# Optimization experiments

Hardware: AMD Instinct MI355X
Metric: run time of the kernel (lower is better)

The kernel has to match this reference:

```python
import math
import jax, jax.numpy as jnp
import numpy as np

B, S, D, H = 2, 2048, 1024, 16
DH = D // H
EPS = 1e-5


def setup_inputs() -> dict:
    key = jax.random.key(0)
    ks = jax.random.split(key, 8)
    def lin(k, din, dout):
        return jax.random.normal(k, (din, dout), dtype=jnp.float32) / math.sqrt(din)
    return {
        "x": jax.random.normal(ks[0], (B, S, D), dtype=jnp.float32),
        "attention_mask": jnp.ones((B, S), dtype=jnp.int32),
        "Wq": lin(ks[1], D, D),
        "Wk": lin(ks[2], D, D),
        "Wv": lin(ks[3], D, D),
        "Wo": lin(ks[4], D, D),
        "W1": lin(ks[5], D, 4 * D),
        "W2": lin(ks[6], 2 * D, D),
        "gamma1": jnp.ones((D,), jnp.float32),
        "beta1": jnp.zeros((D,), jnp.float32),
        "gamma2": jnp.ones((D,), jnp.float32),
        "beta2": jnp.zeros((D,), jnp.float32),
    }


def layernorm(x, gamma, beta):
    mu = jnp.mean(x, axis=-1, keepdims=True)
    xc = x - mu
    var = jnp.mean(xc * xc, axis=-1, keepdims=True)
    return gamma * (xc / jnp.sqrt(var + EPS)) + beta


def softmax_last(x):
    x = x - jnp.max(x, axis=-1, keepdims=True)
    e = jnp.exp(x)
    return e / jnp.sum(e, axis=-1, keepdims=True)


def mhsa(x, attention_mask, Wq, Wk, Wv, Wo, causal=True):
    b, s, d = x.shape
    q = (x @ Wq).reshape(b, s, H, DH).transpose(0, 2, 1, 3)  # [b,h,s,dh]
    k = (x @ Wk).reshape(b, s, H, DH).transpose(0, 2, 1, 3)
    v = (x @ Wv).reshape(b, s, H, DH).transpose(0, 2, 1, 3)
    score = jnp.einsum("bhqd,bhkd->bhqk", q, k) / math.sqrt(DH)
    if causal:
        cmask = jnp.tril(jnp.ones((s, s), dtype=bool))
        score = jnp.where(cmask[None, None], score, -jnp.inf)
    key_mask = attention_mask.astype(bool)[:, None, None, :]  # [b,1,1,s]
    score = jnp.where(key_mask, score, -jnp.inf)
    attn = softmax_last(score)
    out = jnp.einsum("bhqk,bhkd->bhqd", attn, v)
    out = out.transpose(0, 2, 1, 3).reshape(b, s, d)
    return out @ Wo


def reference(x, attention_mask, Wq, Wk, Wv, Wo, W1, W2, gamma1, beta1, gamma2, beta2):
    x1 = x + mhsa(layernorm(x, gamma1, beta1), attention_mask, Wq, Wk, Wv, Wo, causal=True)
    h = layernorm(x1, gamma2, beta2) @ W1          # [b,s,4d]
    left, right = h[:, :, : 2 * D], h[:, :, 2 * D :]
    glu = left * jax.nn.sigmoid(right)             # [b,s,2d]
    return x1 + glu @ W2
```

## Files before the change

### kernel.cpp

```cpp
#include <hip/hip_runtime.h>
#include <hip/hip_bf16.h>
#include <math.h>

#define BB 2
#define SS 2048
#define DD 1024
#define HH 16
#define DH 64
#define NTOK (BB * SS)
#define LN_EPS 1e-5f
#define BIGNEG -1e30f

typedef __attribute__((ext_vector_type(8))) short bf16x8;
typedef __attribute__((ext_vector_type(4))) float f32x4;

static __device__ __forceinline__ unsigned short f2bu(float f) {
    __hip_bfloat16 h = __float2bfloat16(f);
    return *(unsigned short*)&h;
}

static __device__ __forceinline__ float fast_exp2(float x) {
    return __builtin_amdgcn_exp2f(x);
}

static __device__ __forceinline__ void async16(const void* g, void* l) {
    __builtin_amdgcn_global_load_lds((const __attribute__((address_space(1))) void*)g,
                                     (__attribute__((address_space(3))) void*)l, 16, 0, 0);
}


__global__ __launch_bounds__(256) void prep_kernel(const float* __restrict__ Wq,
                                                   const float* __restrict__ Wk,
                                                   const float* __restrict__ Wv,
                                                   const float* __restrict__ Wo,
                                                   const float* __restrict__ W1,
                                                   const float* __restrict__ W2,
                                                   __hip_bfloat16* __restrict__ wqkvt,
                                                   __hip_bfloat16* __restrict__ wot,
                                                   __hip_bfloat16* __restrict__ w1t,
                                                   __hip_bfloat16* __restrict__ w2t,
                                                   const float* __restrict__ x,
                                                   const float* __restrict__ gamma,
                                                   const float* __restrict__ beta,
                                                   __hip_bfloat16* __restrict__ lnb) {
    __shared__ float t[32][33];
    __shared__ float red[256];
    const int bid = blockIdx.x;
    const int tid = threadIdx.x;

    if (bid >= 10240) {
        const int row = bid - 10240;
        const float* xp = x + (size_t)row * DD;
        float vals[4];
        float s = 0.f;
#pragma unroll
        for (int i = 0; i < 4; ++i) {
            float v = xp[tid + i * 256];
            vals[i] = v;
            s += v;
        }
        red[tid] = s;
        __syncthreads();
        for (int st = 128; st > 0; st >>= 1) {
            if (tid < st) red[tid] += red[tid + st];
            __syncthreads();
        }
        const float mu = red[0] * (1.0f / DD);
        __syncthreads();
        float sq = 0.f;
#pragma unroll
        for (int i = 0; i < 4; ++i) {
            float d = vals[i] - mu;
            sq += d * d;
        }
        red[tid] = sq;
        __syncthreads();
        for (int st = 128; st > 0; st >>= 1) {
            if (tid < st) red[tid] += red[tid + st];
            __syncthreads();
        }
        const float rinv = rsqrtf(red[0] * (1.0f / DD) + LN_EPS);
        __hip_bfloat16* op = lnb + (size_t)row * DD;
#pragma unroll
        for (int i = 0; i < 4; ++i) {
            int j = tid + i * 256;
            op[j] = __float2bfloat16(gamma[j] * ((vals[i] - mu) * rinv) + beta[j]);
        }
        return;
    }

    const float* W;
    __hip_bfloat16* Wt;
    int K, N, tile;
    if (bid < 4096) {
        const int m = bid >> 10;
        tile = bid & 1023;
        W = (m == 0) ? Wq : (m == 1) ? Wk : (m == 2) ? Wv : Wo;
        Wt = (m < 3) ? (wqkvt + (size_t)m * 1024 * 1024) : wot;
        K = 1024; N = 1024;
    } else if (bid < 8192) {
        tile = bid - 4096; W = W1; Wt = w1t; K = 1024; N = 4096;
    } else {
        tile = bid - 8192; W = W2; Wt = w2t; K = 2048; N = 1024;
    }
    const int nt = N >> 5;
    const int n0 = (tile % nt) * 32, k0 = (tile / nt) * 32;
    const int tx = tid & 31, ty = tid >> 5;
#pragma unroll
    for (int i = 0; i < 4; ++i)
        t[ty + 8 * i][tx] = W[(size_t)(k0 + ty + 8 * i) * N + n0 + tx];
    __syncthreads();
#pragma unroll
    for (int i = 0; i < 4; ++i)
        Wt[(size_t)(n0 + ty + 8 * i) * K + k0 + tx] = __float2bfloat16(t[tx][ty + 8 * i]);
}

__global__ __launch_bounds__(256) void ln_kernel(const float* __restrict__ x,
                                                 const float* __restrict__ gamma,
                                                 const float* __restrict__ beta,
                                                 __hip_bfloat16* __restrict__ out) {
    const int row = blockIdx.x;
    const int tid = threadIdx.x;
    __shared__ float red[256];

    const float* xp = x + (size_t)row * DD;
    float vals[4];
    float s = 0.f;
#pragma unroll
    for (int i = 0; i < 4; ++i) {
        float v = xp[tid + i * 256];
        vals[i] = v;
        s += v;
    }
    red[tid] = s;
    __syncthreads();
    for (int st = 128; st > 0; st >>= 1) {
        if (tid < st) red[tid] += red[tid + st];
        __syncthreads();
    }
    const float mu = red[0] * (1.0f / DD);
    __syncthreads();
    float sq = 0.f;
#pragma unroll
    for (int i = 0; i < 4; ++i) {
        float d = vals[i] - mu;
        sq += d * d;
    }
    red[tid] = sq;
    __syncthreads();
    for (int st = 128; st > 0; st >>= 1) {
        if (tid < st) red[tid] += red[tid + st];
        __syncthreads();
    }
    const float rinv = rsqrtf(red[0] * (1.0f / DD) + LN_EPS);

    __hip_bfloat16* op = out + (size_t)row * DD;
#pragma unroll
    for (int i = 0; i < 4; ++i) {
        int j = tid + i * 256;
        op[j] = __float2bfloat16(gamma[j] * ((vals[i] - mu) * rinv) + beta[j]);
    }
}

template <int RES, int EPI>
__global__ __launch_bounds__(256) void mfma_gemm(const __hip_bfloat16* __restrict__ A,
                                                 const __hip_bfloat16* __restrict__ Bt,
                                                 const void* __restrict__ res,
                                                 void* __restrict__ out,
                                                 int M, int N, int K,
                                                 int xcdCols, int colGroups,
                                                 __hip_bfloat16* __restrict__ vtout) {
    __shared__ short As[128 * 64];
    __shared__ short Bs[128 * 64];
    const int tid = threadIdx.x;
    const int lane = tid & 63;
    const int wave = tid >> 6;
    const int xcd = blockIdx.x & 7;
    const int i = blockIdx.x >> 3;
    const int xcdRows = (gridDim.x >> 3) / xcdCols;
    const int r = i / xcdCols;
    const int c = i - r * xcdCols;
    const int rowg = xcd / colGroups;
    const int colg = xcd - rowg * colGroups;
    const int row0 = (rowg * xcdRows + r) * 128;
    const int col0 = (colg * xcdCols + c) * 128;
    const int wr = (wave >> 1) * 64;
    const int wc = (wave & 1) * 64;
    const int l15 = lane & 15;
    const int quad = lane >> 4;
    const int s7 = l15 & 7;

    f32x4 acc[4][4] = {};

    for (int k0 = 0; k0 < K; k0 += 64) {
#pragma unroll
        for (int rr = 0; rr < 4; ++rr) {
            const int ec = rr * 256 + tid;
            const int ar = ec >> 3, d = ec & 7;
            const int ao = (d ^ (ar & 7)) << 3;
            async16(&A[(size_t)(row0 + ar) * K + k0 + ao], &As[ec << 3]);
            async16(&Bt[(size_t)(col0 + ar) * K + k0 + ao], &Bs[ec << 3]);
        }
        __syncthreads();
#pragma unroll
        for (int kk = 0; kk < 2; ++kk) {
            const int co = (((kk << 2) | quad) ^ s7) << 3;
            bf16x8 af[4], bfr[4];
#pragma unroll
            for (int ii = 0; ii < 4; ++ii)
                af[ii] = *(const bf16x8*)&As[(wr + ii * 16 + l15) * 64 + co];
#pragma unroll
            for (int j = 0; j < 4; ++j)
                bfr[j] = *(const bf16x8*)&Bs[(wc + j * 16 + l15) * 64 + co];
#pragma unroll
            for (int ii = 0; ii < 4; ++ii)
#pragma unroll
                for (int j = 0; j < 4; ++j)
                    acc[ii][j] = __builtin_amdgcn_mfma_f32_16x16x32_bf16(af[ii], bfr[j], acc[ii][j], 0, 0, 0);
        }
        __syncthreads();
    }

    const int r4 = quad * 4;
    if (vtout != nullptr && col0 >= 2048) {
#pragma unroll
        for (int ii = 0; ii < 4; ++ii) {
#pragma unroll
            for (int j = 0; j < 4; ++j) {
                const int cc = col0 + wc + j * 16 + l15 - 2048;
                const int orow0 = row0 + wr + ii * 16 + r4;
                const unsigned long long pk =
                    (unsigned long long)(((unsigned)f2bu(acc[ii][j][3]) << 16) | f2bu(acc[ii][j][2])) << 32 |
                    (((unsigned)f2bu(acc[ii][j][1]) << 16) | f2bu(acc[ii][j][0]));
                *(unsigned long long*)((unsigned short*)vtout + (size_t)cc * 4096 + orow0) = pk;
            }
        }
        return;
    }
#pragma unroll
    for (int ii = 0; ii < 4; ++ii) {
#pragma unroll
        for (int j = 0; j < 4; ++j) {
            const int orow0 = row0 + wr + ii * 16 + r4;
            const int ocol = col0 + wc + j * 16 + l15;
#pragma unroll
            for (int rg = 0; rg < 4; ++rg) {
                const size_t oi = (size_t)(orow0 + rg) * N + ocol;
                float v = acc[ii][j][rg];
                if constexpr (RES == 1) v += ((const float*)res)[oi];
                if constexpr (EPI == 0) ((float*)out)[oi] = v;
                if constexpr (EPI == 1) ((__hip_bfloat16*)out)[oi] = __float2bfloat16(v);
            }
        }
    }
}

template <int RES, int EPI>
__global__ __launch_bounds__(256) void mfma_gemm_n6464(const __hip_bfloat16* __restrict__ A,
                                                       const __hip_bfloat16* __restrict__ Bt,
                                                       const void* __restrict__ res,
                                                       void* __restrict__ out,
                                                       int N, int K) {
    __shared__ short As[64 * 64];
    __shared__ short Bs[64 * 64];
    const int tid = threadIdx.x;
    const int lane = tid & 63;
    const int wave = tid >> 6;
    const int xcd = blockIdx.x & 7;
    const int i = blockIdx.x >> 3;
    const int row0 = ((xcd >> 1) * 16 + (i >> 3)) * 64;
    const int col0 = ((xcd & 1) * 8 + (i & 7)) * 64;
    const int wr = wave * 16;
    const int l15 = lane & 15;
    const int quad = lane >> 4;
    const int s7 = l15 & 7;

    f32x4 acc[4] = {};

    for (int k0 = 0; k0 < K; k0 += 64) {
#pragma unroll
        for (int r = 0; r < 2; ++r) {
            const int ec = r * 256 + tid;
            const int ar = ec >> 3, d = ec & 7;
            const int ao = (d ^ (ar & 7)) << 3;
            async16(&A[(size_t)(row0 + ar) * K + k0 + ao], &As[ec << 3]);
            async16(&Bt[(size_t)(col0 + ar) * K + k0 + ao], &Bs[ec << 3]);
        }
        __syncthreads();
#pragma unroll
        for (int kk = 0; kk < 2; ++kk) {
            const int co = (((kk << 2) | quad) ^ s7) << 3;
            const bf16x8 af = *(const bf16x8*)&As[(wr + l15) * 64 + co];
            bf16x8 bfr[4];
#pragma unroll
            for (int j = 0; j < 4; ++j)
                bfr[j] = *(const bf16x8*)&Bs[(j * 16 + l15) * 64 + co];
#pragma unroll
            for (int j = 0; j < 4; ++j)
                acc[j] = __builtin_amdgcn_mfma_f32_16x16x32_bf16(af, bfr[j], acc[j], 0, 0, 0);
        }
        __syncthreads();
    }

    const int r4 = quad * 4;
#pragma unroll
    for (int j = 0; j < 4; ++j) {
        const int orow0 = row0 + wr + r4;
        const int ocol = col0 + j * 16 + l15;
#pragma unroll
        for (int rg = 0; rg < 4; ++rg) {
            const size_t oi = (size_t)(orow0 + rg) * N + ocol;
            float v = acc[j][rg];
            if constexpr (RES == 1) v += ((const float*)res)[oi];
            if constexpr (EPI == 0) ((float*)out)[oi] = v;
            if constexpr (EPI == 1) ((__hip_bfloat16*)out)[oi] = __float2bfloat16(v);
        }
    }
}

__global__ __launch_bounds__(256) void mfma_gemm_glu3264(const __hip_bfloat16* __restrict__ A,
                                                         const __hip_bfloat16* __restrict__ Bt,
                                                         __hip_bfloat16* __restrict__ out) {
    __shared__ short As[64 * 64];
    __shared__ short Bl[64 * 64];
    __shared__ short Br[64 * 64];
    const int tid = threadIdx.x;
    const int lane = tid & 63;
    const int wave = tid >> 6;
    const int xcd = blockIdx.x & 7;
    const int i = blockIdx.x >> 3;
    const int row0 = ((xcd >> 1) * 16 + (i >> 4)) * 64;
    const int col0 = ((xcd & 1) * 16 + (i & 15)) * 64;
    const int wr = wave * 16;
    const int l15 = lane & 15;
    const int quad = lane >> 4;
    const int s7 = l15 & 7;

    f32x4 accl[4] = {};
    f32x4 accr[4] = {};

    for (int k0 = 0; k0 < 1024; k0 += 64) {
#pragma unroll
        for (int r = 0; r < 2; ++r) {
            const int ec = r * 256 + tid;
            const int ar = ec >> 3, d = ec & 7;
            const int ao = (d ^ (ar & 7)) << 3;
            async16(&A[(size_t)(row0 + ar) * 1024 + k0 + ao], &As[ec << 3]);
            async16(&Bt[(size_t)(col0 + ar) * 1024 + k0 + ao], &Bl[ec << 3]);
            async16(&Bt[(size_t)(2048 + col0 + ar) * 1024 + k0 + ao], &Br[ec << 3]);
        }
        __syncthreads();
#pragma unroll
        for (int kk = 0; kk < 2; ++kk) {
            const int co = (((kk << 2) | quad) ^ s7) << 3;
            const bf16x8 af = *(const bf16x8*)&As[(wr + l15) * 64 + co];
            bf16x8 bl[4], br[4];
#pragma unroll
            for (int j = 0; j < 4; ++j) {
                bl[j] = *(const bf16x8*)&Bl[(j * 16 + l15) * 64 + co];
                br[j] = *(const bf16x8*)&Br[(j * 16 + l15) * 64 + co];
            }
#pragma unroll
            for (int j = 0; j < 4; ++j) {
                accl[j] = __builtin_amdgcn_mfma_f32_16x16x32_bf16(af, bl[j], accl[j], 0, 0, 0);
                accr[j] = __builtin_amdgcn_mfma_f32_16x16x32_bf16(af, br[j], accr[j], 0, 0, 0);
            }
        }
        __syncthreads();
    }

    const int r4 = quad * 4;
#pragma unroll
    for (int j = 0; j < 4; ++j) {
        const int orow0 = row0 + wr + r4;
        const int ocol = col0 + j * 16 + l15;
#pragma unroll
        for (int rg = 0; rg < 4; ++rg) {
            const float l = accl[j][rg];
            const float r = accr[j][rg];
            out[(size_t)(orow0 + rg) * 2048 + ocol] =
                __float2bfloat16(l * (1.f / (1.f + __expf(-r))));
        }
    }
}

#define KADV (64 * 3072)
#define SCL2E 0.1803368801f
#define RESCALE_THR2 11.54f

__global__ __launch_bounds__(256, 4) void flash_mfma(const __hip_bfloat16* __restrict__ qkv_,
                                                     const __hip_bfloat16* __restrict__ VT_,
                                                     const int* __restrict__ mask,
                                                     __hip_bfloat16* __restrict__ attnb) {
    const unsigned short* qkv = (const unsigned short*)qkv_;
    const unsigned short* VT = (const unsigned short*)VT_;
    __shared__ __align__(16) short Ks[2][64 * 64];
    __shared__ __align__(16) short Vt[2][64 * 64];
    __shared__ __align__(16) short Ps[4][16 * 64];

    const int tid = threadIdx.x;
    const int lane = tid & 63;
    const int wave = tid >> 6;
    const int l15 = lane & 15;
    const int quad = lane >> 4;
    const int s7 = l15 & 7;

    const int xcd = blockIdx.x & 7;
    const int slot = blockIdx.x >> 3;
    const int bh = xcd + ((slot & 3) << 3);
    const int v = slot >> 2;
    const int vr = v & 7, vs = v >> 3;
    const int qt = (vs == 0) ? 31 - vr : (vs == 1) ? vr : (vs == 2) ? 23 - vr : 8 + vr;
    const int h = bh & 15;
    const int b = bh >> 4;
    const int q0 = qt * 64 + wave * 16;

    const int e0 = tid, e1 = 256 + tid;
    const int r0 = e0 >> 3, d0 = e0 & 7, r1 = e1 >> 3, d1 = e1 & 7;
    const unsigned short* kp0 = qkv + (size_t)(b * SS + r0) * 3072 + 1024 + h * 64 + ((d0 ^ (r0 & 7)) << 3);
    const unsigned short* kp1 = qkv + (size_t)(b * SS + r1) * 3072 + 1024 + h * 64 + ((d1 ^ (r1 & 7)) << 3);
    const unsigned short* vp0 = VT + (size_t)(h * 64 + r0) * 4096 + b * SS + ((d0 ^ (r0 & 7)) << 3);
    const unsigned short* vp1 = VT + (size_t)(h * 64 + r1) * 4096 + b * SS + ((d1 ^ (r1 & 7)) << 3);
    short* const kd0a = &Ks[0][e0 << 3]; short* const kd0b = &Ks[1][e0 << 3];
    short* const kd1a = &Ks[0][e1 << 3]; short* const kd1b = &Ks[1][e1 << 3];
    short* const vd0a = &Vt[0][e0 << 3]; short* const vd0b = &Vt[1][e0 << 3];
    short* const vd1a = &Vt[0][e1 << 3]; short* const vd1b = &Vt[1][e1 << 3];

    const int* const mrow = mask + b * SS;

    bf16x8 aq[2];
#pragma unroll
    for (int ks = 0; ks < 2; ++ks)
        aq[ks] = *(const bf16x8*)(qkv + (size_t)(b * SS + q0 + l15) * 3072 +
                                  h * 64 + ks * 32 + quad * 8);

    f32x4 O[4];
#pragma unroll
    for (int i = 0; i < 4; ++i) O[i] = (f32x4){0.f, 0.f, 0.f, 0.f};
    float m_r = BIGNEG, l_r = 0.f;

    short* const Pw = &Ps[wave][0];

    async16(kp0, kd0a); async16(kp1, kd1a);
    async16(vp0, vd0a); async16(vp1, vd1a);
    kp0 += KADV; kp1 += KADV; vp0 += 64; vp1 += 64;

    for (int c = 0; c < qt; ++c) {
        const int cur = c & 1;
        __syncthreads();

        async16(kp0, cur ? kd0a : kd0b);
        async16(kp1, cur ? kd1a : kd1b);
        async16(vp0, cur ? vd0a : vd0b);
        async16(vp1, cur ? vd1a : vd1b);
        kp0 += KADV; kp1 += KADV; vp0 += 64; vp1 += 64;

        const int kb = c << 6;
        const short* Kc = &Ks[cur][0];
        const short* Vc = &Vt[cur][0];

        int4 mv[4];
#pragma unroll
        for (int kt = 0; kt < 4; ++kt)
            mv[kt] = *(const int4*)&mrow[kb + kt * 16 + quad * 4];

        f32x4 S[4];
        __builtin_amdgcn_s_setprio(1);
#pragma unroll
        for (int kt = 0; kt < 4; ++kt) {
            const bf16x8 bk0 = *(const bf16x8*)&Kc[(kt * 16 + l15) * 64 + ((quad ^ s7) << 3)];
            const bf16x8 bk1 = *(const bf16x8*)&Kc[(kt * 16 + l15) * 64 + (((4 | quad) ^ s7) << 3)];
            f32x4 z = {0.f, 0.f, 0.f, 0.f};
            z = __builtin_amdgcn_mfma_f32_16x16x32_bf16(bk0, aq[0], z, 0, 0, 0);
            S[kt] = __builtin_amdgcn_mfma_f32_16x16x32_bf16(bk1, aq[1], z, 0, 0, 0);
        }
        __builtin_amdgcn_s_setprio(0);

#pragma unroll
        for (int kt = 0; kt < 4; ++kt) {
            const int* mm = (const int*)&mv[kt];
#pragma unroll
            for (int rg = 0; rg < 4; ++rg)
                S[kt][rg] = fmaf(S[kt][rg], SCL2E, mm[rg] ? 0.f : BIGNEG);
        }

        const float t0 = fmaxf(fmaxf(S[0][0], S[0][1]), fmaxf(S[0][2], S[0][3]));
        const float t1 = fmaxf(fmaxf(S[1][0], S[1][1]), fmaxf(S[1][2], S[1][3]));
        const float t2 = fmaxf(fmaxf(S[2][0], S[2][1]), fmaxf(S[2][2], S[2][3]));
        const float t3 = fmaxf(fmaxf(S[3][0], S[3][1]), fmaxf(S[3][2], S[3][3]));
        float tmax = fmaxf(fmaxf(t0, t1), fmaxf(t2, t3));
        tmax = fmaxf(tmax, __shfl_xor(tmax, 16));
        tmax = fmaxf(tmax, __shfl_xor(tmax, 32));

        if (__any(tmax > m_r + RESCALE_THR2)) {
            const float mn = fmaxf(m_r, tmax);
            const float alpha = fast_exp2(m_r - mn);
            m_r = mn;
            l_r *= alpha;
#pragma unroll
            for (int nt = 0; nt < 4; ++nt)
#pragma unroll
                for (int rg = 0; rg < 4; ++rg)
                    O[nt][rg] *= alpha;
        }

        float rsum = 0.f;
        unsigned long long p64[4];
#pragma unroll
        for (int kt = 0; kt < 4; ++kt) {
#pragma unroll
            for (int rg = 0; rg < 4; ++rg)
                S[kt][rg] = fast_exp2(S[kt][rg] - m_r);
            rsum += (S[kt][0] + S[kt][1]) + (S[kt][2] + S[kt][3]);
            p64[kt] = ((unsigned long long)(((unsigned)f2bu(S[kt][3]) << 16) | f2bu(S[kt][2])) << 32)
                    | (((unsigned)f2bu(S[kt][1]) << 16) | f2bu(S[kt][0]));
        }
        rsum += __shfl_xor(rsum, 16);
        rsum += __shfl_xor(rsum, 32);
        l_r += rsum;

#pragma unroll
        for (int kt = 0; kt < 4; ++kt) {
            const int ch = (kt << 1) | (quad >> 1);
            const int base = (l15 << 6) + ((ch ^ s7) << 3) + ((quad & 1) << 2);
            *(unsigned long long*)&Pw[base] = p64[kt];
        }

        __builtin_amdgcn_s_setprio(1);
#pragma unroll
        for (int kk = 0; kk < 2; ++kk) {
            const int co = ((((kk << 2) | quad) ^ s7) << 3);
            const bf16x8 bp = *(const bf16x8*)&Pw[(l15 << 6) + co];
#pragma unroll
            for (int nt = 0; nt < 4; ++nt) {
                const bf16x8 av = *(const bf16x8*)&Vc[(nt * 16 + l15) * 64 + co];
                O[nt] = __builtin_amdgcn_mfma_f32_16x16x32_bf16(av, bp, O[nt], 0, 0, 0);
            }
        }
        __builtin_amdgcn_s_setprio(0);
    }

    {
        const int cur = qt & 1;
        __syncthreads();

        const int kb = qt << 6;
        const int ktmax = wave + 1;
        const int ktfull = wave;
        const short* Kc = &Ks[cur][0];
        const short* Vc = &Vt[cur][0];
        const int qrow = q0 + l15;

        int4 mv[4];
#pragma unroll
        for (int kt = 0; kt < 4; ++kt) {
            if (kt >= ktmax) break;
            mv[kt] = *(const int4*)&mrow[kb + kt * 16 + quad * 4];
        }

        f32x4 S[4];
        __builtin_amdgcn_s_setprio(1);
#pragma unroll
        for (int kt = 0; kt < 4; ++kt) {
            if (kt >= ktmax) break;
            const bf16x8 bk0 = *(const bf16x8*)&Kc[(kt * 16 + l15) * 64 + ((quad ^ s7) << 3)];
            const bf16x8 bk1 = *(const bf16x8*)&Kc[(kt * 16 + l15) * 64 + (((4 | quad) ^ s7) << 3)];
            f32x4 z = {0.f, 0.f, 0.f, 0.f};
            z = __builtin_amdgcn_mfma_f32_16x16x32_bf16(bk0, aq[0], z, 0, 0, 0);
            S[kt] = __builtin_amdgcn_mfma_f32_16x16x32_bf16(bk1, aq[1], z, 0, 0, 0);
        }
        __builtin_amdgcn_s_setprio(0);

#pragma unroll
        for (int kt = 0; kt < 4; ++kt) {
            if (kt >= ktmax) break;
            const int* mm = (const int*)&mv[kt];
#pragma unroll
            for (int rg = 0; rg < 4; ++rg) {
                float s = fmaf(S[kt][rg], SCL2E, mm[rg] ? 0.f : BIGNEG);
                if (kt >= ktfull) {
                    const int key = kb + kt * 16 + quad * 4 + rg;
                    s = (key <= qrow) ? s : BIGNEG;
                }
                S[kt][rg] = s;
            }
        }

        float tmax = BIGNEG;
#pragma unroll
        for (int kt = 0; kt < 4; ++kt) {
            if (kt >= ktmax) break;
            tmax = fmaxf(tmax, fmaxf(fmaxf(S[kt][0], S[kt][1]),
                                     fmaxf(S[kt][2], S[kt][3])));
        }
        tmax = fmaxf(tmax, __shfl_xor(tmax, 16));
        tmax = fmaxf(tmax, __shfl_xor(tmax, 32));

        if (__any(tmax > m_r + RESCALE_THR2)) {
            const float mn = fmaxf(m_r, tmax);
            const float alpha = fast_exp2(m_r - mn);
            m_r = mn;
            l_r *= alpha;
#pragma unroll
            for (int nt = 0; nt < 4; ++nt)
#pragma unroll
                for (int rg = 0; rg < 4; ++rg)
                    O[nt][rg] *= alpha;
        }

        float rsum = 0.f;
#pragma unroll
        for (int kt = 0; kt < 4; ++kt) {
            if (kt >= ktmax) break;
#pragma unroll
            for (int rg = 0; rg < 4; ++rg)
                S[kt][rg] = fast_exp2(S[kt][rg] - m_r);
            rsum += (S[kt][0] + S[kt][1]) + (S[kt][2] + S[kt][3]);
            const int ch = (kt << 1) | (quad >> 1);
            const int base = (l15 << 6) + ((ch ^ s7) << 3) + ((quad & 1) << 2);
            *(unsigned long long*)&Pw[base] =
                ((unsigned long long)(((unsigned)f2bu(S[kt][3]) << 16) | f2bu(S[kt][2])) << 32)
                | (((unsigned)f2bu(S[kt][1]) << 16) | f2bu(S[kt][0]));
        }
        rsum += __shfl_xor(rsum, 16);
        rsum += __shfl_xor(rsum, 32);
        l_r += rsum;

        const int kkmax = (ktmax + 1) >> 1;
        if (ktmax & 1) {
            const int ch = (ktmax << 1) | (quad >> 1);
            const int base = (l15 << 6) + ((ch ^ s7) << 3) + ((quad & 1) << 2);
            *(unsigned long long*)&Pw[base] = 0ull;
        }

        __builtin_amdgcn_s_setprio(1);
#pragma unroll
        for (int kk = 0; kk < 2; ++kk) {
            if (kk >= kkmax) break;
            const int co = ((((kk << 2) | quad) ^ s7) << 3);
            const bf16x8 bp = *(const bf16x8*)&Pw[(l15 << 6) + co];
#pragma unroll
            for (int nt = 0; nt < 4; ++nt) {
                const bf16x8 av = *(const bf16x8*)&Vc[(nt * 16 + l15) * 64 + co];
                O[nt] = __builtin_amdgcn_mfma_f32_16x16x32_bf16(av, bp, O[nt], 0, 0, 0);
            }
        }
        __builtin_amdgcn_s_setprio(0);
    }

    const float inv = 1.f / l_r;
    unsigned short* op = (unsigned short*)attnb +
                         (size_t)(b * SS + q0 + l15) * 1024 + h * 64 + quad * 4;
#pragma unroll
    for (int nt = 0; nt < 4; ++nt) {
        const float o0 = O[nt][0] * inv, o1 = O[nt][1] * inv;
        const float o2 = O[nt][2] * inv, o3 = O[nt][3] * inv;
        const unsigned long long pk =
            (unsigned long long)(((unsigned)f2bu(o3) << 16) | f2bu(o2)) << 32 |
            (((unsigned)f2bu(o1) << 16) | f2bu(o0));
        *(unsigned long long*)(op + nt * 16) = pk;
    }
}

extern "C" void kernel_launch(void* const* d_in, const int* in_sizes, int n_in,
                              void* d_out, int out_size, void* d_ws, size_t ws_size,
                              hipStream_t stream) {
    const float* x  = (const float*)d_in[0];
    const int* mask = (const int*)d_in[1];
    const float* Wq = (const float*)d_in[2];
    const float* Wk = (const float*)d_in[3];
    const float* Wv = (const float*)d_in[4];
    const float* Wo = (const float*)d_in[5];
    const float* W1 = (const float*)d_in[6];
    const float* W2 = (const float*)d_in[7];
    const float* g1 = (const float*)d_in[8];
    const float* b1 = (const float*)d_in[9];
    const float* g2 = (const float*)d_in[10];
    const float* b2 = (const float*)d_in[11];

    const size_t MB = 1024 * 1024;
    uint8_t* ws = (uint8_t*)d_ws;
    __hip_bfloat16* wqkvt = (__hip_bfloat16*)(ws);
    __hip_bfloat16* wot   = (__hip_bfloat16*)(ws + 6 * MB);
    __hip_bfloat16* w1t   = (__hip_bfloat16*)(ws + 8 * MB);
    __hip_bfloat16* w2t   = (__hip_bfloat16*)(ws + 16 * MB);
    __hip_bfloat16* lnb   = (__hip_bfloat16*)(ws + 20 * MB);
    __hip_bfloat16* qkvb  = (__hip_bfloat16*)(ws + 28 * MB);
    float*          x1    = (float*)(ws + 28 * MB);
    __hip_bfloat16* attnb = (__hip_bfloat16*)(ws + 52 * MB);
    __hip_bfloat16* VT    = (__hip_bfloat16*)(ws + 60 * MB);
    __hip_bfloat16* glub  = (__hip_bfloat16*)(ws + 68 * MB);

    prep_kernel<<<10240 + NTOK, 256, 0, stream>>>(Wq, Wk, Wv, Wo, W1, W2,
                                                  wqkvt, wot, w1t, w2t,
                                                  x, g1, b1, lnb);

    mfma_gemm<0, 1><<<768, 256, 0, stream>>>(lnb, wqkvt, nullptr, qkvb,
                                             NTOK, 3072, 1024, 12, 2, VT);

    flash_mfma<<<1024, 256, 0, stream>>>(qkvb, VT, mask, attnb);

    mfma_gemm_n6464<1, 0><<<1024, 256, 0, stream>>>(attnb, wot, x, x1, 1024, 1024);

    ln_kernel<<<NTOK, 256, 0, stream>>>(x1, g2, b2, lnb);

    mfma_gemm_glu3264<<<2048, 256, 0, stream>>>(lnb, w1t, glub);

    mfma_gemm_n6464<1, 0><<<1024, 256, 0, stream>>>(glub, w2t, x1, (float*)d_out,
                                                    1024, 2048);
}
```

Baseline: 188.4 us.

## Double flash attention query tile to 128 rows with 8 waves per block

The flash attention kernel now uses 512-thread blocks covering 128 query rows, with 8 waves each handling 16 rows, so every K/V tile loaded into LDS is shared by twice as many queries. Each thread now issues one async copy per tile instead of two. The causal diagonal is handled by a generic loop over the last two 64-key chunks, with per-wave masked-tile counts. This halves the grid and coarsens causal load balancing, which can hurt tail behaviour and occupancy.

After: 195.5 us. 3.8% more time.

```diff
diff --git a/kernel.cpp b/kernel.cpp
--- a/kernel.cpp
+++ b/kernel.cpp
@@ -388,7 +388,7 @@
 #define SCL2E 0.1803368801f
 #define RESCALE_THR2 11.54f
 
-__global__ __launch_bounds__(256, 4) void flash_mfma(const __hip_bfloat16* __restrict__ qkv_,
+__global__ __launch_bounds__(512, 4) void flash_mfma(const __hip_bfloat16* __restrict__ qkv_,
                                                      const __hip_bfloat16* __restrict__ VT_,
                                                      const int* __restrict__ mask,
                                                      __hip_bfloat16* __restrict__ attnb) {
@@ -396,7 +396,7 @@
     const unsigned short* VT = (const unsigned short*)VT_;
     __shared__ __align__(16) short Ks[2][64 * 64];
     __shared__ __align__(16) short Vt[2][64 * 64];
-    __shared__ __align__(16) short Ps[4][16 * 64];
+    __shared__ __align__(16) short Ps[8][16 * 64];
 
     const int tid = threadIdx.x;
     const int lane = tid & 63;
@@ -410,21 +410,16 @@
     const int bh = xcd + ((slot & 3) << 3);
     const int v = slot >> 2;
     const int vr = v & 7, vs = v >> 3;
-    const int qt = (vs == 0) ? 31 - vr : (vs == 1) ? vr : (vs == 2) ? 23 - vr : 8 + vr;
+    const int qt2 = vs ? vr : 15 - vr;
     const int h = bh & 15;
     const int b = bh >> 4;
-    const int q0 = qt * 64 + wave * 16;
-
-    const int e0 = tid, e1 = 256 + tid;
-    const int r0 = e0 >> 3, d0 = e0 & 7, r1 = e1 >> 3, d1 = e1 & 7;
+    const int q0 = qt2 * 128 + wave * 16;
+
+    const int r0 = tid >> 3, d0 = tid & 7;
     const unsigned short* kp0 = qkv + (size_t)(b * SS + r0) * 3072 + 1024 + h * 64 + ((d0 ^ (r0 & 7)) << 3);
-    const unsigned short* kp1 = qkv + (size_t)(b * SS + r1) * 3072 + 1024 + h * 64 + ((d1 ^ (r1 & 7)) << 3);
     const unsigned short* vp0 = VT + (size_t)(h * 64 + r0) * 4096 + b * SS + ((d0 ^ (r0 & 7)) << 3);
-    const unsigned short* vp1 = VT + (size_t)(h * 64 + r1) * 4096 + b * SS + ((d1 ^ (r1 & 7)) << 3);
-    short* const kd0a = &Ks[0][e0 << 3]; short* const kd0b = &Ks[1][e0 << 3];
-    short* const kd1a = &Ks[0][e1 << 3]; short* const kd1b = &Ks[1][e1 << 3];
-    short* const vd0a = &Vt[0][e0 << 3]; short* const vd0b = &Vt[1][e0 << 3];
-    short* const vd1a = &Vt[0][e1 << 3]; short* const vd1b = &Vt[1][e1 << 3];
+    short* const kd0a = &Ks[0][tid << 3]; short* const kd0b = &Ks[1][tid << 3];
+    short* const vd0a = &Vt[0][tid << 3]; short* const vd0b = &Vt[1][tid << 3];
 
     const int* const mrow = mask + b * SS;
 
@@ -441,19 +436,20 @@
 
     short* const Pw = &Ps[wave][0];
 
-    async16(kp0, kd0a); async16(kp1, kd1a);
-    async16(vp0, vd0a); async16(vp1, vd1a);
-    kp0 += KADV; kp1 += KADV; vp0 += 64; vp1 += 64;
-
-    for (int c = 0; c < qt; ++c) {
+    const int nch = 2 * qt2 + 2;
+    const int fullEnd = 2 * qt2;
+
+    async16(kp0, kd0a);
+    async16(vp0, vd0a);
+    kp0 += KADV; vp0 += 64;
+
+    for (int c = 0; c < fullEnd; ++c) {
         const int cur = c & 1;
         __syncthreads();
 
         async16(kp0, cur ? kd0a : kd0b);
-        async16(kp1, cur ? kd1a : kd1b);
         async16(vp0, cur ? vd0a : vd0b);
-        async16(vp1, cur ? vd1a : vd1b);
-        kp0 += KADV; kp1 += KADV; vp0 += 64; vp1 += 64;
+        kp0 += KADV; vp0 += 64;
 
         const int kb = c << 6;
         const short* Kc = &Ks[cur][0];
@@ -540,13 +536,24 @@
         __builtin_amdgcn_s_setprio(0);
     }
 
-    {
-        const int cur = qt & 1;
-        __syncthreads();
-
-        const int kb = qt << 6;
-        const int ktmax = wave + 1;
-        const int ktfull = wave;
+    for (int c = fullEnd; c < nch; ++c) {
+        const int cur = c & 1;
+        __syncthreads();
+
+        if (c + 1 < nch) {
+            async16(kp0, cur ? kd0a : kd0b);
+            async16(vp0, cur ? vd0a : vd0b);
+            kp0 += KADV; vp0 += 64;
+        }
+
+        const int kb = c << 6;
+        const int dq = q0 - kb;
+        if (dq + 15 < 0) continue;
+
+        int ktmax = ((dq + 15) >> 4) + 1;
+        if (ktmax > 4) ktmax = 4;
+        int ktfull = (dq - 15) >= 0 ? ((dq - 15) >> 4) + 1 : 0;
+        if (ktfull > 4) ktfull = 4;
         const short* Kc = &Ks[cur][0];
         const short* Vc = &Vt[cur][0];
         const int qrow = q0 + l15;
@@ -698,7 +705,7 @@
     mfma_gemm<0, 1><<<768, 256, 0, stream>>>(lnb, wqkvt, nullptr, qkvb,
                                              NTOK, 3072, 1024, 12, 2, VT);
 
-    flash_mfma<<<1024, 256, 0, stream>>>(qkvb, VT, mask, attnb);
+    flash_mfma<<<512, 512, 0, stream>>>(qkvb, VT, mask, attnb);
 
     mfma_gemm_n6464<1, 0><<<1024, 256, 0, stream>>>(attnb, wot, x, x1, 1024, 1024);
 
```
